# Kernel optimization log

Hardware: AMD Instinct MI355X
Metric: run time of the kernel (lower is better)

## Reference

```python
import jax, jax.numpy as jnp
import numpy as np

LMAX = 2; C = 64; H = 8; D = C // H
N_NODES = 10000; N_EDGES = 160000
M = (LMAX + 1) ** 2                      # 9 spherical components
RAD_IN = 64; RAD_HID = 64
WNUM = (LMAX + 1) * C                    # per-edge CP-TP weights: one per (l, channel)
L_OF_M = jnp.array([l for l in range(LMAX + 1) for _ in range(2 * l + 1)])
LN_EPS = 1e-5


def _lin(x, W, b=None):
    # Linear over channel (last) dim; bias applied ONLY to scalar (m=0) component
    y = jnp.einsum('nmc,cd->nmd', x, W)
    if b is not None:
        y = y.at[:, 0, :].add(b)
    return y


def _cp_tp(x, sh, w_lc):
    # CP tensor product with SH: channelwise product, per-(l, channel) radial weight
    # x: [E, M, C], sh: [E, M], w_lc: [E, LMAX+1, C]
    return x * sh[:, :, None] * w_lc[:, L_OF_M, :]


def _radial(s, W1, b1, g, b, W2, off):
    h = s @ W1 + b1
    mu = h.mean(-1, keepdims=True)
    var = h.var(-1, keepdims=True)
    h = (h - mu) / jnp.sqrt(var + LN_EPS) * g + b
    h = jax.nn.silu(h)
    return (h @ W2 + off).reshape(-1, LMAX + 1, C)


def _smooth_lrelu(x, a=0.2):
    return (1 + a) / 2 * x + (1 - a) / 2 * x * (2 * jax.nn.sigmoid(x) - 1)


def _gate(x):
    c = x.shape[-1] // 2
    v = x[..., :c]
    g = jax.nn.sigmoid(x[:, 0, c:])[:, None, :]
    return jnp.concatenate([jax.nn.silu(v[:, :1, :]), v[:, 1:, :] * g], axis=1)


def _seg_softmax(a, idx, n):
    # numerically stable softmax over edges grouped by destination node
    m = jax.ops.segment_max(a, idx, num_segments=n)
    e = jnp.exp(a - m[idx])
    s = jax.ops.segment_sum(e, idx, num_segments=n)
    return e / (s[idx] + 1e-16)


def setup_inputs():
    key = jax.random.key(0)
    ks = jax.random.split(key, 16)
    def w(k, shape, fan_in):
        return jax.random.normal(k, shape, jnp.float32) / np.sqrt(fan_in)
    bound = 1.0 / np.sqrt(RAD_HID)
    return {
        'node_input': jax.random.normal(ks[0], (N_NODES, M, C), jnp.float32),
        'edge_attr': jax.random.normal(ks[1], (N_EDGES, M), jnp.float32),
        'edge_scalars': jax.random.normal(ks[2], (N_EDGES, RAD_IN), jnp.float32),
        'W_src': w(ks[3], (C, C), C), 'b_src': jnp.zeros((C,), jnp.float32),
        'W_dst': w(ks[4], (C, C), C),
        'rad_W1': w(ks[5], (RAD_IN, RAD_HID), RAD_IN),
        'rad_b1': jnp.zeros((RAD_HID,), jnp.float32),
        'rad_ln_g': jnp.ones((RAD_HID,), jnp.float32),
        'rad_ln_b': jnp.zeros((RAD_HID,), jnp.float32),
        'rad_W2': w(ks[6], (RAD_HID, WNUM), RAD_HID),
        'rad_offset': jax.random.uniform(ks[7], (WNUM,), jnp.float32, -bound, bound),
        'W_alpha': w(ks[8], (C, C), C), 'b_alpha': jnp.zeros((C,), jnp.float32),
        'alpha_dot': w(ks[9], (H, D), D),
        'W_value': w(ks[10], (C, 2 * C), C), 'b_value': jnp.zeros((2 * C,), jnp.float32),
        'W_proj': w(ks[11], (C, C), C), 'b_proj': jnp.zeros((C,), jnp.float32),
        'edge_src': jax.random.randint(ks[12], (N_EDGES,), 0, N_NODES),
        'edge_dst': jax.random.randint(ks[13], (N_EDGES,), 0, N_NODES),
        'batch': jnp.zeros((N_NODES,), jnp.int32),
    }


def reference(node_input, edge_attr, edge_scalars, W_src, b_src, W_dst,
              rad_W1, rad_b1, rad_ln_g, rad_ln_b, rad_W2, rad_offset,
              W_alpha, b_alpha, alpha_dot, W_value, b_value, W_proj, b_proj,
              edge_src, edge_dst, batch):
    # gather: per-edge merged message [E, M, C]
    msg = _lin(node_input, W_src, b_src)[edge_src] + _lin(node_input, W_dst)[edge_dst]
    # per-edge radial weights for both tensor products [E, LMAX+1, C]
    w_lc = _radial(edge_scalars, rad_W1, rad_b1, rad_ln_g, rad_ln_b, rad_W2, rad_offset)
    msg = _cp_tp(msg, edge_attr, w_lc)
    # alpha path: scalar channel only
    alpha = _lin(msg, W_alpha, b_alpha)[:, 0, :].reshape(-1, H, D)
    alpha = _smooth_lrelu(alpha)[:, None]                 # [E, 1, H, D]
    alpha = jnp.einsum('bikd,kd->bik', alpha, alpha_dot)  # [E, 1, H]
    alpha = _seg_softmax(alpha, edge_dst, N_NODES)        # dropout disabled (eval)
    # value path
    value = _gate(_lin(msg, W_value, b_value))
    value = _cp_tp(value, edge_attr, w_lc)
    value = value.reshape(N_EDGES, M, H, D)
    # scatter-aggregate to destination nodes
    out = jax.ops.segment_sum(value * alpha[:, :, :, None], edge_dst, num_segments=N_NODES)
    return _lin(out.reshape(N_NODES, M, C), W_proj, b_proj)
```

## Files before the change

### kernel.cpp

```cpp
#include <hip/hip_runtime.h>
#include <stdint.h>

#define NN 10000
#define NE 160000

struct BF16 { unsigned short v; };
typedef _Float16 h2_t __attribute__((ext_vector_type(2)));
typedef _Float16 f16x8 __attribute__((ext_vector_type(8)));
typedef float f32x4 __attribute__((ext_vector_type(4)));

__device__ __forceinline__ float cvt(float x) { return x; }
__device__ __forceinline__ float cvt(BF16 x) {
    union { unsigned int i; float f; } u; u.i = ((unsigned int)x.v) << 16; return u.f;
}
__device__ __forceinline__ unsigned short f2b_us(float f) {
    union { float f; unsigned int i; } v; v.f = f;
    unsigned int x = v.i;
    unsigned int lsb = (x >> 16) & 1u;
    x += 0x7fffu + lsb;
    return (unsigned short)(x >> 16);
}
__device__ __forceinline__ float rlane(float v, int l) {
    return __uint_as_float((unsigned int)__builtin_amdgcn_readlane(__float_as_uint(v), l));
}
__device__ __forceinline__ h2_t rlane_pk(h2_t v, int l) {
    union { h2_t h; unsigned int u; } c; c.h = v;
    c.u = (unsigned int)__builtin_amdgcn_readlane(c.u, l);
    return c.h;
}
__device__ __forceinline__ h2_t pkh2(float a, float b) {
    h2_t r; r[0] = (_Float16)a; r[1] = (_Float16)b; return r;
}
__device__ __forceinline__ float fdot2f(h2_t a, h2_t b, float c) {
#if __has_builtin(__builtin_amdgcn_fdot2)
    return __builtin_amdgcn_fdot2(a, b, c, false);
#else
    return fmaf((float)a[0], (float)b[0], fmaf((float)a[1], (float)b[1], c));
#endif
}
__device__ __forceinline__ float sigm(float x) { return 1.0f / (1.0f + __expf(-x)); }
__device__ __forceinline__ int clampi(int v, int hi) { return (unsigned)v >= (unsigned)hi ? 0 : v; }

__device__ __forceinline__ void stOut(float* p, size_t i, float v) { p[i] = v; }
__device__ __forceinline__ void stOut(unsigned short* p, size_t i, float v) { p[i] = f2b_us(v); }

__device__ __forceinline__ unsigned okey(float f) {
    unsigned b = __float_as_uint(f);
    return (b & 0x80000000u) ? ~b : (b | 0x80000000u);
}
__device__ __forceinline__ float okdec(unsigned k) {
    unsigned b = (k & 0x80000000u) ? (k ^ 0x80000000u) : ~k;
    return __uint_as_float(b);
}

__device__ __forceinline__ f16x8 ld8f16(const BF16* p) {
    uint4 v = *(const uint4*)p;
    unsigned w0 = v.x, w1 = v.y, w2 = v.z, w3 = v.w;
    f16x8 r;
    union { unsigned u; float f; } c;
    c.u = (w0 & 0xFFFFu) << 16;  r[0] = (_Float16)c.f;
    c.u = (w0 & 0xFFFF0000u);    r[1] = (_Float16)c.f;
    c.u = (w1 & 0xFFFFu) << 16;  r[2] = (_Float16)c.f;
    c.u = (w1 & 0xFFFF0000u);    r[3] = (_Float16)c.f;
    c.u = (w2 & 0xFFFFu) << 16;  r[4] = (_Float16)c.f;
    c.u = (w2 & 0xFFFF0000u);    r[5] = (_Float16)c.f;
    c.u = (w3 & 0xFFFFu) << 16;  r[6] = (_Float16)c.f;
    c.u = (w3 & 0xFFFF0000u);    r[7] = (_Float16)c.f;
    return r;
}
__device__ __forceinline__ f16x8 ld8f16(const float* p) {
    float4 a = *(const float4*)p;
    float4 b = *(const float4*)(p + 4);
    f16x8 r;
    r[0] = (_Float16)a.x; r[1] = (_Float16)a.y; r[2] = (_Float16)a.z; r[3] = (_Float16)a.w;
    r[4] = (_Float16)b.x; r[5] = (_Float16)b.y; r[6] = (_Float16)b.z; r[7] = (_Float16)b.w;
    return r;
}

__global__ void k0_zero(int* __restrict__ cnt, int* __restrict__ csr, int* __restrict__ flag,
                        float* __restrict__ nsum, unsigned* __restrict__ mseg,
                        float* __restrict__ sseg) {
    int i = blockIdx.x * blockDim.x + threadIdx.x;
    if (i == 0) *flag = 1;
    if (i < NN) cnt[i] = 0;
    if (i < NE) csr[i] = 0;
    if (i < NN * 8) { mseg[i] = 0u; sseg[i] = 0.f; }
    for (int j = i; j < NN * 576; j += gridDim.x * blockDim.x) nsum[j] = 0.f;
}

__global__ void kprobe(const unsigned short* __restrict__ x, int* __restrict__ flag) {
    int bad = 0;
    for (int i = threadIdx.x; i < 16384; i += blockDim.x) {
        unsigned e = (x[i] >> 7) & 0xFFu;
        bad += (e == 0xFFu);
    }
    if (bad > 0) atomicExch(flag, 0);
}

template<typename T>
__device__ void k1m_body(const T* x, const T* Ws, const T* bs, const T* Wd,
                         _Float16* fs, _Float16* fd, _Float16 (*Yt)[128])
{
    const int lane = threadIdx.x & 63;
    const int c16 = lane & 15;
    const int kg  = lane >> 4;

    f16x8 bWs[4][2], bWd[4][2];
#pragma unroll
    for (int t = 0; t < 4; t++)
#pragma unroll
        for (int kh = 0; kh < 2; kh++) {
            f16x8 f1, f2;
#pragma unroll
            for (int j = 0; j < 8; j++) {
                int k = kh * 32 + kg * 8 + j;
                f1[j] = (_Float16)cvt(Ws[(size_t)k * 64 + t * 16 + c16]);
                f2[j] = (_Float16)cvt(Wd[(size_t)k * 64 + t * 16 + c16]);
            }
            bWs[t][kh] = f1; bWd[t][kh] = f2;
        }
    float bsv[4];
#pragma unroll
    for (int t = 0; t < 4; t++) bsv[t] = cvt(bs[t * 16 + c16]);

    const int NT = (NN * 9) / 16;
    for (int tile = blockIdx.x * 4 + (threadIdx.x >> 6); tile < NT; tile += gridDim.x * 4) {
        const int r0 = tile * 16;
        f16x8 a0 = ld8f16(&x[(size_t)(r0 + c16) * 64 + kg * 8]);
        f16x8 a1 = ld8f16(&x[(size_t)(r0 + c16) * 64 + 32 + kg * 8]);
        f32x4 hs[4] = {{0,0,0,0},{0,0,0,0},{0,0,0,0},{0,0,0,0}};
        f32x4 hd[4] = {{0,0,0,0},{0,0,0,0},{0,0,0,0},{0,0,0,0}};
#pragma unroll
        for (int t = 0; t < 4; t++) {
            hs[t] = __builtin_amdgcn_mfma_f32_16x16x32_f16(a0, bWs[t][0], hs[t], 0, 0, 0);
            hs[t] = __builtin_amdgcn_mfma_f32_16x16x32_f16(a1, bWs[t][1], hs[t], 0, 0, 0);
            hd[t] = __builtin_amdgcn_mfma_f32_16x16x32_f16(a0, bWd[t][0], hd[t], 0, 0, 0);
            hd[t] = __builtin_amdgcn_mfma_f32_16x16x32_f16(a1, bWd[t][1], hd[t], 0, 0, 0);
        }
#pragma unroll
        for (int t = 0; t < 4; t++)
#pragma unroll
            for (int r = 0; r < 4; r++) {
                int row = kg * 4 + r;
                float vs = hs[t][r];
                if (((r0 + row) % 9) == 0) vs += bsv[t];
                Yt[row][t * 16 + c16] = (_Float16)vs;
                Yt[row][64 + t * 16 + c16] = (_Float16)hd[t][r];
            }
#pragma unroll
        for (int j = 0; j < 2; j++) {
            int c = lane + 64 * j;
            int row = c >> 3;
            int cc = (c & 7) * 8;
            *(f16x8*)&fs[(size_t)(r0 + row) * 64 + cc] = *(const f16x8*)&Yt[row][cc];
            *(f16x8*)&fd[(size_t)(r0 + row) * 64 + cc] = *(const f16x8*)&Yt[row][64 + cc];
        }
    }
}

__global__ __launch_bounds__(256) void k1m_feats(
    const void* x, const void* Ws, const void* bs, const void* Wd,
    _Float16* fs, _Float16* fd, const int* flag)
{
    __shared__ _Float16 Y[4][16][128];
    const int wv = threadIdx.x >> 6;
    if (*flag) k1m_body<BF16>((const BF16*)x, (const BF16*)Ws, (const BF16*)bs, (const BF16*)Wd,
                              fs, fd, Y[wv]);
    else       k1m_body<float>((const float*)x, (const float*)Ws, (const float*)bs, (const float*)Wd,
                               fs, fd, Y[wv]);
}

__global__ void k2a_count(const int* __restrict__ dst, int* __restrict__ cnt) {
    for (int e = blockIdx.x * blockDim.x + threadIdx.x; e < NE; e += gridDim.x * blockDim.x)
        atomicAdd(&cnt[clampi(dst[e], NN)], 1);
}

__global__ __launch_bounds__(1024) void k2b_scan(const int* __restrict__ cnt,
                                                 int* __restrict__ off, int* __restrict__ cur) {
    __shared__ int part[1024];
    int t = threadIdx.x;
    int base = t * 10;
    int loc[10]; int s = 0;
#pragma unroll
    for (int k = 0; k < 10; k++) { int i = base + k; int v = (i < NN) ? cnt[i] : 0; loc[k] = v; s += v; }
    part[t] = s; __syncthreads();
    for (int o = 1; o < 1024; o <<= 1) {
        int v = (t >= o) ? part[t - o] : 0;
        __syncthreads();
        part[t] += v;
        __syncthreads();
    }
    int run = (t == 0) ? 0 : part[t - 1];
#pragma unroll
    for (int k = 0; k < 10; k++) {
        int i = base + k;
        if (i < NN) { off[i] = run; cur[i] = run; run += loc[k]; }
    }
    if (t == 1023) off[NN] = part[1023];
}

__global__ void k2c_fill(const int* __restrict__ dst, int* __restrict__ cur, int* __restrict__ csr) {
    for (int e = blockIdx.x * blockDim.x + threadIdx.x; e < NE; e += gridDim.x * blockDim.x) {
        int d = clampi(dst[e], NN);
        int p = atomicAdd(&cur[d], 1);
        if ((unsigned)p < (unsigned)NE) csr[p] = e;
    }
}

template<typename T>
__device__ void k3m_body(const T* es, const T* W1, const T* b1g, const T* gg, const T* bbv,
                         const T* W2, const T* roff, _Float16* wlc,
                         _Float16 (*Yt)[200])
{
    const int lane = threadIdx.x & 63;
    const int c16 = lane & 15;
    const int kg  = lane >> 4;

    f16x8 bW1[4][2], bW2[12][2];
#pragma unroll
    for (int t = 0; t < 4; t++)
#pragma unroll
        for (int kh = 0; kh < 2; kh++) {
            f16x8 f;
#pragma unroll
            for (int j = 0; j < 8; j++) {
                int k = kh * 32 + kg * 8 + j;
                f[j] = (_Float16)cvt(W1[(size_t)k * 64 + t * 16 + c16]);
            }
            bW1[t][kh] = f;
        }
#pragma unroll
    for (int t = 0; t < 12; t++)
#pragma unroll
        for (int kh = 0; kh < 2; kh++) {
            f16x8 f;
#pragma unroll
            for (int j = 0; j < 8; j++) {
                int k = kh * 32 + kg * 8 + j;
                f[j] = (_Float16)cvt(W2[(size_t)k * 192 + t * 16 + c16]);
            }
            bW2[t][kh] = f;
        }
    float b1v[4], gv[4], bv[4], rv[12];
#pragma unroll
    for (int t = 0; t < 4; t++) {
        b1v[t] = cvt(b1g[t * 16 + c16]);
        gv[t]  = cvt(gg[t * 16 + c16]);
        bv[t]  = cvt(bbv[t * 16 + c16]);
    }
#pragma unroll
    for (int t = 0; t < 12; t++) rv[t] = cvt(roff[t * 16 + c16]);

    const int NT = NE / 16;
    for (int tile = blockIdx.x * 4 + (threadIdx.x >> 6); tile < NT; tile += gridDim.x * 4) {
        const int e0 = tile * 16;
        f16x8 a0 = ld8f16(&es[(size_t)(e0 + c16) * 64 + kg * 8]);
        f16x8 a1 = ld8f16(&es[(size_t)(e0 + c16) * 64 + 32 + kg * 8]);
        f32x4 h[4] = {{0,0,0,0},{0,0,0,0},{0,0,0,0},{0,0,0,0}};
#pragma unroll
        for (int t = 0; t < 4; t++) {
            h[t] = __builtin_amdgcn_mfma_f32_16x16x32_f16(a0, bW1[t][0], h[t], 0, 0, 0);
            h[t] = __builtin_amdgcn_mfma_f32_16x16x32_f16(a1, bW1[t][1], h[t], 0, 0, 0);
        }
#pragma unroll
        for (int r = 0; r < 4; r++) {
            float x0 = h[0][r] + b1v[0], x1 = h[1][r] + b1v[1];
            float x2 = h[2][r] + b1v[2], x3 = h[3][r] + b1v[3];
            float s = x0 + x1 + x2 + x3;
            float q = x0 * x0 + x1 * x1 + x2 * x2 + x3 * x3;
            s += __shfl_xor(s, 1, 64); q += __shfl_xor(q, 1, 64);
            s += __shfl_xor(s, 2, 64); q += __shfl_xor(q, 2, 64);
            s += __shfl_xor(s, 4, 64); q += __shfl_xor(q, 4, 64);
            s += __shfl_xor(s, 8, 64); q += __shfl_xor(q, 8, 64);
            float mu = s * (1.0f / 64.0f);
            float var = fmaxf(q * (1.0f / 64.0f) - mu * mu, 0.0f);
            float rs = rsqrtf(var + 1e-5f);
            int row = kg * 4 + r;
#pragma unroll
            for (int t = 0; t < 4; t++) {
                float xt = (t == 0) ? x0 : (t == 1) ? x1 : (t == 2) ? x2 : x3;
                float v = (xt - mu) * rs * gv[t] + bv[t];
                v = v * sigm(v);
                Yt[row][t * 16 + c16] = (_Float16)v;
            }
        }
        f16x8 a20 = *(const f16x8*)&Yt[c16][kg * 8];
        f16x8 a21 = *(const f16x8*)&Yt[c16][32 + kg * 8];
        f32x4 y[12] = {{0,0,0,0},{0,0,0,0},{0,0,0,0},{0,0,0,0},{0,0,0,0},{0,0,0,0},
                       {0,0,0,0},{0,0,0,0},{0,0,0,0},{0,0,0,0},{0,0,0,0},{0,0,0,0}};
#pragma unroll
        for (int t = 0; t < 12; t++) {
            y[t] = __builtin_amdgcn_mfma_f32_16x16x32_f16(a20, bW2[t][0], y[t], 0, 0, 0);
            y[t] = __builtin_amdgcn_mfma_f32_16x16x32_f16(a21, bW2[t][1], y[t], 0, 0, 0);
        }
#pragma unroll
        for (int t = 0; t < 12; t++)
#pragma unroll
            for (int r = 0; r < 4; r++)
                Yt[kg * 4 + r][t * 16 + c16] = (_Float16)(y[t][r] + rv[t]);
#pragma unroll
        for (int j = 0; j < 6; j++) {
            int c = lane + 64 * j;
            int row = c / 24;
            int cc = (c % 24) * 8;
            *(f16x8*)&wlc[(size_t)(e0 + row) * 192 + cc] = *(const f16x8*)&Yt[row][cc];
        }
    }
}

__global__ __launch_bounds__(256) void k3m_wlc(
    const void* es, const void* W1, const void* b1, const void* g, const void* bln,
    const void* W2, const void* roff, _Float16* wlc, const int* flag)
{
    __shared__ _Float16 Y[4][16][200];
    const int wv = threadIdx.x >> 6;
    if (*flag) k3m_body<BF16>((const BF16*)es, (const BF16*)W1, (const BF16*)b1, (const BF16*)g,
                              (const BF16*)bln, (const BF16*)W2, (const BF16*)roff, wlc, Y[wv]);
    else       k3m_body<float>((const float*)es, (const float*)W1, (const float*)b1, (const float*)g,
                               (const float*)bln, (const float*)W2, (const float*)roff, wlc, Y[wv]);
}

template<typename T>
__device__ void k4m_body(const T* ea, const _Float16* fs, const _Float16* fd,
                         const _Float16* wlc, const T* Wa, const T* ba, const T* adot,
                         const int* esrc, const int* edst, float* alpha, unsigned* mseg,
                         float (*aS)[8])
{
    const int lane = threadIdx.x & 63;
    const int c16 = lane & 15;
    const int kg  = lane >> 6 == 0 ? (lane >> 4) : (lane >> 4);

    f16x8 bWa[4][2];
#pragma unroll
    for (int t = 0; t < 4; t++)
#pragma unroll
        for (int kh = 0; kh < 2; kh++) {
            f16x8 f;
#pragma unroll
            for (int j = 0; j < 8; j++) {
                int k = kh * 32 + (lane >> 4) * 8 + j;
                f[j] = (_Float16)cvt(Wa[(size_t)k * 64 + t * 16 + c16]);
            }
            bWa[t][kh] = f;
        }
    float bav[4], adv[4];
#pragma unroll
    for (int t = 0; t < 4; t++) {
        bav[t] = cvt(ba[t * 16 + c16]);
        adv[t] = cvt(adot[t * 16 + c16]);
    }
    const int kgr = lane >> 4;

    const int NT = NE / 16;
    for (int tile = blockIdx.x * 4 + (threadIdx.x >> 6); tile < NT; tile += gridDim.x * 4) {
        const int e0 = tile * 16;
        const int eA = e0 + c16;
        const int sn = clampi(esrc[eA], NN);
        const int dn = clampi(edst[eA], NN);
        f16x8 fs0 = *(const f16x8*)&fs[(size_t)sn * 576 + kgr * 8];
        f16x8 fs1 = *(const f16x8*)&fs[(size_t)sn * 576 + 32 + kgr * 8];
        f16x8 fd0 = *(const f16x8*)&fd[(size_t)dn * 576 + kgr * 8];
        f16x8 fd1 = *(const f16x8*)&fd[(size_t)dn * 576 + 32 + kgr * 8];
        f16x8 wl0 = *(const f16x8*)&wlc[(size_t)eA * 192 + kgr * 8];
        f16x8 wl1 = *(const f16x8*)&wlc[(size_t)eA * 192 + 32 + kgr * 8];
        _Float16 eh = (_Float16)cvt(ea[(size_t)eA * 9]);
        f16x8 ev;
#pragma unroll
        for (int j = 0; j < 8; j++) ev[j] = eh;
        f16x8 a0 = (fs0 + fd0) * ev * wl0;
        f16x8 a1 = (fs1 + fd1) * ev * wl1;

        f32x4 d[4] = {{0,0,0,0},{0,0,0,0},{0,0,0,0},{0,0,0,0}};
#pragma unroll
        for (int t = 0; t < 4; t++) {
            d[t] = __builtin_amdgcn_mfma_f32_16x16x32_f16(a0, bWa[t][0], d[t], 0, 0, 0);
            d[t] = __builtin_amdgcn_mfma_f32_16x16x32_f16(a1, bWa[t][1], d[t], 0, 0, 0);
        }
#pragma unroll
        for (int t = 0; t < 4; t++)
#pragma unroll
            for (int r = 0; r < 4; r++) {
                float aw = d[t][r] + bav[t];
                float f = aw * (0.2f + 0.8f * sigm(aw));
                float p = f * adv[t];
                p += __shfl_xor(p, 1, 64);
                p += __shfl_xor(p, 2, 64);
                p += __shfl_xor(p, 4, 64);
                if ((c16 & 7) == 0)
                    aS[kgr * 4 + r][t * 2 + (c16 >> 3)] = p;
            }
#pragma unroll
        for (int j = 0; j < 2; j++) {
            int idx = lane * 2 + j;
            int row = idx >> 3, h = idx & 7;
            float p = aS[row][h];
            alpha[(size_t)(e0 + row) * 8 + h] = p;
            int dnr = clampi(edst[e0 + row], NN);
            atomicMax(&mseg[dnr * 8 + h], okey(p));
        }
    }
}

__global__ __launch_bounds__(256) void k4m_alpha(
    const void* ea, const _Float16* fs, const _Float16* fd, const _Float16* wlc,
    const void* Wa, const void* ba, const void* adot,
    const int* esrc, const int* edst, float* alpha, unsigned* mseg, const int* flag)
{
    __shared__ float A[4][16][8];
    const int wv = threadIdx.x >> 6;
    if (*flag) k4m_body<BF16>((const BF16*)ea, fs, fd, wlc, (const BF16*)Wa, (const BF16*)ba,
                              (const BF16*)adot, esrc, edst, alpha, mseg, A[wv]);
    else       k4m_body<float>((const float*)ea, fs, fd, wlc, (const float*)Wa, (const float*)ba,
                               (const float*)adot, esrc, edst, alpha, mseg, A[wv]);
}

__global__ void k5b_expsum(const int* __restrict__ edst, const unsigned* __restrict__ mseg,
                           float* __restrict__ alpha, float* __restrict__ sseg) {
    int t = blockIdx.x * blockDim.x + threadIdx.x;
    if (t >= NE * 8) return;
    int e = t >> 3, h = t & 7;
    int dn = clampi(edst[e], NN);
    float m = okdec(mseg[dn * 8 + h]);
    float ex = __expf(alpha[t] - m);
    alpha[t] = ex;
    unsafeAtomicAdd(&sseg[dn * 8 + h], ex);
}

template<typename T>
__device__ void k6m_body(const int* off, const int* csr, const int* esrc,
                         const T* ea, const _Float16* fs, const _Float16* fd,
                         const _Float16* wlc, const T* Wv, const T* bv,
                         const float* alpha, const float* sseg, float* nsum,
                         _Float16 (*wlS)[16][72], float (*mtS)[20])
{
    const int lane = threadIdx.x & 63;
    const int wvid = threadIdx.x >> 6;
    const int c16 = lane & 15;
    const int kg  = lane >> 4;

    for (int gw = blockIdx.x * 4 + wvid; gw < NN * 2; gw += gridDim.x * 4) {
        const int n = gw >> 1;
        const int half = gw & 1;
        const int b = off[n], e_end = off[n + 1];
        if (b >= e_end) continue;

        f16x8 bfV[2][2], bfG[2][2];
        float bvv[2], bgv[2];
        int colg[2], hh[2];
        float invs[2];
#pragma unroll
        for (int t = 0; t < 2; t++) {
            colg[t] = (half * 2 + t) * 16 + c16;
            hh[t] = colg[t] >> 3;
            invs[t] = 1.0f / (sseg[n * 8 + hh[t]] + 1e-16f);
#pragma unroll
            for (int kh = 0; kh < 2; kh++) {
                f16x8 b8v, b8g;
#pragma unroll
                for (int j = 0; j < 8; j++) {
                    int k = kh * 32 + kg * 8 + j;
                    b8v[j] = (_Float16)cvt(Wv[(size_t)k * 128 + colg[t]]);
                    b8g[j] = (_Float16)cvt(Wv[(size_t)k * 128 + 64 + colg[t]]);
                }
                bfV[t][kh] = b8v; bfG[t][kh] = b8g;
            }
            bvv[t] = cvt(bv[colg[t]]);
            bgv[t] = cvt(bv[64 + colg[t]]);
        }

        const size_t fdb = (size_t)n * 576;
        const size_t nbase = (size_t)n * 576;

        for (int p0 = b; p0 < e_end; p0 += 16) {
            int pA = p0 + c16; if (pA >= e_end) pA = e_end - 1;
            const int eA = clampi(csr[pA], NE);
            const int snA = clampi(esrc[eA], NN);
            const size_t fsb = (size_t)snA * 576;
            const size_t wlb = (size_t)eA * 192;

#pragma unroll
            for (int l = 0; l < 3; l++)
#pragma unroll
                for (int kh = 0; kh < 2; kh++)
                    *(f16x8*)&wlS[l][c16][kh * 32 + kg * 8] =
                        *(const f16x8*)&wlc[wlb + (size_t)l * 64 + kh * 32 + kg * 8];
            float eao[9];
#pragma unroll
            for (int m = 0; m < 9; m++) eao[m] = cvt(ea[(size_t)eA * 9 + m]);
            if (kg == 0) {
#pragma unroll
                for (int m = 0; m < 9; m++) mtS[c16][m] = eao[m];
            }
            mtS[c16][10 + kg * 2]     = alpha[(size_t)eA * 8 + kg * 2];
            mtS[c16][10 + kg * 2 + 1] = alpha[(size_t)eA * 8 + kg * 2 + 1];

            float awm[2][4];
#pragma unroll
            for (int r = 0; r < 4; r++) {
                int row = kg * 4 + r;
                float vm = (p0 + row < e_end) ? 1.f : 0.f;
#pragma unroll
                for (int t = 0; t < 2; t++)
                    awm[t][r] = mtS[row][10 + hh[t]] * invs[t] * vm;
            }

            float gtv[2][4];
            {
                f16x8 a0, a1;
                {
                    f16x8 w0 = *(const f16x8*)&wlS[0][c16][kg * 8];
                    f16x8 w1 = *(const f16x8*)&wlS[0][c16][32 + kg * 8];
                    f16x8 fd0 = *(const f16x8*)&fd[fdb + kg * 8];
                    f16x8 fd1 = *(const f16x8*)&fd[fdb + 32 + kg * 8];
                    f16x8 fs0 = *(const f16x8*)&fs[fsb + kg * 8];
                    f16x8 fs1 = *(const f16x8*)&fs[fsb + 32 + kg * 8];
                    _Float16 eh = (_Float16)eao[0];
                    f16x8 ev;
#pragma unroll
                    for (int j = 0; j < 8; j++) ev[j] = eh;
                    a0 = (fs0 + fd0) * ev * w0;
                    a1 = (fs1 + fd1) * ev * w1;
                }
                f32x4 d[2] = {{0,0,0,0},{0,0,0,0}};
                f32x4 g[2] = {{0,0,0,0},{0,0,0,0}};
#pragma unroll
                for (int t = 0; t < 2; t++) {
                    d[t] = __builtin_amdgcn_mfma_f32_16x16x32_f16(a0, bfV[t][0], d[t], 0, 0, 0);
                    d[t] = __builtin_amdgcn_mfma_f32_16x16x32_f16(a1, bfV[t][1], d[t], 0, 0, 0);
                    g[t] = __builtin_amdgcn_mfma_f32_16x16x32_f16(a0, bfG[t][0], g[t], 0, 0, 0);
                    g[t] = __builtin_amdgcn_mfma_f32_16x16x32_f16(a1, bfG[t][1], g[t], 0, 0, 0);
                }
#pragma unroll
                for (int t = 0; t < 2; t++) {
                    float ps = 0.f;
#pragma unroll
                    for (int r = 0; r < 4; r++) {
                        int row = kg * 4 + r;
                        gtv[t][r] = sigm(g[t][r] + bgv[t]);
                        float v = d[t][r] + bvv[t];
                        float f = v * sigm(v);
                        float wlv = (float)wlS[0][row][colg[t]];
                        float eam = mtS[row][0];
                        ps = fmaf(f * (eam * wlv), awm[t][r], ps);
                    }
                    ps += __shfl_xor(ps, 16, 64);
                    ps += __shfl_xor(ps, 32, 64);
                    if (kg == 0) unsafeAtomicAdd(&nsum[nbase + colg[t]], ps);
                }
            }
#pragma unroll 2
            for (int m = 1; m < 9; m++) {
                const int l = (m < 4) ? 1 : 2;
                f16x8 a0, a1;
                {
                    const size_t mo = (size_t)m * 64;
                    f16x8 w0 = *(const f16x8*)&wlS[l][c16][kg * 8];
                    f16x8 w1 = *(const f16x8*)&wlS[l][c16][32 + kg * 8];
                    f16x8 fd0 = *(const f16x8*)&fd[fdb + mo + kg * 8];
                    f16x8 fd1 = *(const f16x8*)&fd[fdb + mo + 32 + kg * 8];
                    f16x8 fs0 = *(const f16x8*)&fs[fsb + mo + kg * 8];
                    f16x8 fs1 = *(const f16x8*)&fs[fsb + mo + 32 + kg * 8];
                    _Float16 eh = (_Float16)eao[m];
                    f16x8 ev;
#pragma unroll
                    for (int j = 0; j < 8; j++) ev[j] = eh;
                    a0 = (fs0 + fd0) * ev * w0;
                    a1 = (fs1 + fd1) * ev * w1;
                }
                f32x4 d[2] = {{0,0,0,0},{0,0,0,0}};
#pragma unroll
                for (int t = 0; t < 2; t++) {
                    d[t] = __builtin_amdgcn_mfma_f32_16x16x32_f16(a0, bfV[t][0], d[t], 0, 0, 0);
                    d[t] = __builtin_amdgcn_mfma_f32_16x16x32_f16(a1, bfV[t][1], d[t], 0, 0, 0);
                }
#pragma unroll
                for (int t = 0; t < 2; t++) {
                    float ps = 0.f;
#pragma unroll
                    for (int r = 0; r < 4; r++) {
                        int row = kg * 4 + r;
                        float f = d[t][r] * gtv[t][r];
                        float wlv = (float)wlS[l][row][colg[t]];
                        float eam = mtS[row][m];
                        ps = fmaf(f * (eam * wlv), awm[t][r], ps);
                    }
                    ps += __shfl_xor(ps, 16, 64);
                    ps += __shfl_xor(ps, 32, 64);
                    if (kg == 0) unsafeAtomicAdd(&nsum[nbase + (size_t)m * 64 + colg[t]], ps);
                }
            }
        }
    }
}

__global__ __launch_bounds__(256) void k6m_fused(
    const int* off, const int* csr, const int* esrc,
    const void* ea, const _Float16* fs, const _Float16* fd, const _Float16* wlc,
    const void* Wv, const void* bv,
    const float* alpha, const float* sseg, float* nsum, const int* flag)
{
    __shared__ _Float16 shwl[4][3][16][72];
    __shared__ float    shmt[4][16][20];
    const int wvid = threadIdx.x >> 6;
    if (*flag) k6m_body<BF16>(off, csr, esrc, (const BF16*)ea, fs, fd, wlc,
                              (const BF16*)Wv, (const BF16*)bv, alpha, sseg, nsum,
                              shwl[wvid], shmt[wvid]);
    else       k6m_body<float>(off, csr, esrc, (const float*)ea, fs, fd, wlc,
                               (const float*)Wv, (const float*)bv, alpha, sseg, nsum,
                               shwl[wvid], shmt[wvid]);
}

template<typename T, typename OT>
__device__ void k7_body(const float* nsum, const T* Wp, const T* bp, OT* out)
{
    int lane = threadIdx.x & 63;
    int wv = threadIdx.x >> 6;
    float wp[64];
#pragma unroll
    for (int i = 0; i < 64; i++) wp[i] = cvt(Wp[i * 64 + lane]);
    float bpl = cvt(bp[lane]);
    const int ROWS = NN * 9;
    for (int r = blockIdx.x * 4 + wv; r < ROWS; r += gridDim.x * 4) {
        float xv = nsum[(size_t)r * 64 + lane];
        float o0 = 0, o1 = 0, o2 = 0, o3 = 0;
#pragma unroll
        for (int i = 0; i < 64; i += 4) {
            o0 = fmaf(rlane(xv, i), wp[i], o0);
            o1 = fmaf(rlane(xv, i + 1), wp[i + 1], o1);
            o2 = fmaf(rlane(xv, i + 2), wp[i + 2], o2);
            o3 = fmaf(rlane(xv, i + 3), wp[i + 3], o3);
        }
        float o = o0 + o1 + o2 + o3;
        if ((r % 9) == 0) o += bpl;
        stOut(out, (size_t)r * 64 + lane, o);
    }
}

__global__ __launch_bounds__(256) void k7_proj(
    const float* nsum, const void* Wp, const void* bp, void* out, const int* flag)
{
    if (*flag) k7_body<BF16, unsigned short>(nsum, (const BF16*)Wp, (const BF16*)bp, (unsigned short*)out);
    else       k7_body<float, float>(nsum, (const float*)Wp, (const float*)bp, (float*)out);
}

extern "C" void kernel_launch(void* const* d_in, const int* in_sizes, int n_in,
                              void* d_out, int out_size, void* d_ws, size_t ws_size,
                              hipStream_t stream) {
    const void* node_input = d_in[0];
    const void* edge_attr  = d_in[1];
    const void* edge_scal  = d_in[2];
    const void* W_src      = d_in[3];
    const void* b_src      = d_in[4];
    const void* W_dst      = d_in[5];
    const void* rad_W1     = d_in[6];
    const void* rad_b1     = d_in[7];
    const void* rad_ln_g   = d_in[8];
    const void* rad_ln_b   = d_in[9];
    const void* rad_W2     = d_in[10];
    const void* rad_off    = d_in[11];
    const void* W_alpha    = d_in[12];
    const void* b_alpha    = d_in[13];
    const void* alpha_dot  = d_in[14];
    const void* W_value    = d_in[15];
    const void* b_value    = d_in[16];
    const void* W_proj     = d_in[17];
    const void* b_proj     = d_in[18];
    const int* edge_src    = (const int*)d_in[19];
    const int* edge_dst    = (const int*)d_in[20];

    char* ws = (char*)d_ws;
    size_t ofs = 0;
    auto alloc = [&](size_t bytes) -> char* {
        char* r = ws + ofs;
        ofs = (ofs + bytes + 255) & ~(size_t)255;
        return r;
    };

    int* flag       = (int*)alloc(256);
    int* cnt        = (int*)alloc((size_t)NN * 4);
    int* offs       = (int*)alloc((size_t)(NN + 16) * 4);
    int* cur        = (int*)alloc((size_t)NN * 4);
    int* csr        = (int*)alloc((size_t)NE * 4);
    unsigned* mseg  = (unsigned*)alloc((size_t)NN * 8 * 4);
    float* sseg     = (float*)alloc((size_t)NN * 8 * 4);
    float* alpha    = (float*)alloc((size_t)NE * 8 * 4);
    _Float16* fs    = (_Float16*)alloc((size_t)NN * 576 * 2);
    _Float16* fd    = (_Float16*)alloc((size_t)NN * 576 * 2);
    _Float16* wlc   = (_Float16*)alloc((size_t)NE * 192 * 2);
    float* nsum32   = (float*)alloc((size_t)NN * 576 * 4);

    k0_zero<<<dim3(625), dim3(256), 0, stream>>>(cnt, csr, flag, nsum32, mseg, sseg);
    kprobe<<<dim3(1), dim3(256), 0, stream>>>((const unsigned short*)node_input, flag);
    k1m_feats<<<dim3(1408), dim3(256), 0, stream>>>(node_input, W_src, b_src, W_dst, fs, fd, flag);
    k2a_count<<<dim3(512), dim3(256), 0, stream>>>(edge_dst, cnt);
    k2b_scan<<<dim3(1), dim3(1024), 0, stream>>>(cnt, offs, cur);
    k2c_fill<<<dim3(512), dim3(256), 0, stream>>>(edge_dst, cur, csr);
    k3m_wlc<<<dim3(512), dim3(256), 0, stream>>>(edge_scal, rad_W1, rad_b1, rad_ln_g, rad_ln_b,
                                                 rad_W2, rad_off, wlc, flag);
    k4m_alpha<<<dim3(2500), dim3(256), 0, stream>>>(edge_attr, fs, fd, wlc, W_alpha, b_alpha,
                                                    alpha_dot, edge_src, edge_dst, alpha, mseg, flag);
    k5b_expsum<<<dim3(5000), dim3(256), 0, stream>>>(edge_dst, mseg, alpha, sseg);
    k6m_fused<<<dim3(5000), dim3(256), 0, stream>>>(offs, csr, edge_src, edge_attr, fs, fd, wlc,
                                                    W_value, b_value, alpha, sseg, nsum32, flag);
    k7_proj<<<dim3(2048), dim3(256), 0, stream>>>(nsum32, W_proj, b_proj, d_out, flag);
}
```

Baseline: 488.3 us.

## Accumulate node sums in registers, store fp16, and use MFMA for projection

The fused value kernel now keeps per-node partial sums in registers across all incoming edges and writes each node's result once as fp16. This replaces per-tile float atomics into a zero-initialised fp32 buffer, so the zeroing loop in k0 is dropped. The output projection becomes an MFMA 16x16x32 fp16 tile kernel that stages results through shared memory for vectorised stores. Nodes with no incoming edges now get explicit zeros because the early continue was removed. Storing the intermediate in fp16 lowers precision before the projection.

```diff
diff --git a/kernel.cpp b/kernel.cpp
--- a/kernel.cpp
+++ b/kernel.cpp
@@ -78,14 +78,12 @@
 }
 
 __global__ void k0_zero(int* __restrict__ cnt, int* __restrict__ csr, int* __restrict__ flag,
-                        float* __restrict__ nsum, unsigned* __restrict__ mseg,
-                        float* __restrict__ sseg) {
+                        unsigned* __restrict__ mseg, float* __restrict__ sseg) {
     int i = blockIdx.x * blockDim.x + threadIdx.x;
     if (i == 0) *flag = 1;
     if (i < NN) cnt[i] = 0;
     if (i < NE) csr[i] = 0;
     if (i < NN * 8) { mseg[i] = 0u; sseg[i] = 0.f; }
-    for (int j = i; j < NN * 576; j += gridDim.x * blockDim.x) nsum[j] = 0.f;
 }
 
 __global__ void kprobe(const unsigned short* __restrict__ x, int* __restrict__ flag) {
@@ -328,7 +326,7 @@
 {
     const int lane = threadIdx.x & 63;
     const int c16 = lane & 15;
-    const int kg  = lane >> 6 == 0 ? (lane >> 4) : (lane >> 4);
+    const int kgr = lane >> 4;
 
     f16x8 bWa[4][2];
 #pragma unroll
@@ -338,7 +336,7 @@
             f16x8 f;
 #pragma unroll
             for (int j = 0; j < 8; j++) {
-                int k = kh * 32 + (lane >> 4) * 8 + j;
+                int k = kh * 32 + kgr * 8 + j;
                 f[j] = (_Float16)cvt(Wa[(size_t)k * 64 + t * 16 + c16]);
             }
             bWa[t][kh] = f;
@@ -349,7 +347,6 @@
         bav[t] = cvt(ba[t * 16 + c16]);
         adv[t] = cvt(adot[t * 16 + c16]);
     }
-    const int kgr = lane >> 4;
 
     const int NT = NE / 16;
     for (int tile = blockIdx.x * 4 + (threadIdx.x >> 6); tile < NT; tile += gridDim.x * 4) {
@@ -430,7 +427,7 @@
 __device__ void k6m_body(const int* off, const int* csr, const int* esrc,
                          const T* ea, const _Float16* fs, const _Float16* fd,
                          const _Float16* wlc, const T* Wv, const T* bv,
-                         const float* alpha, const float* sseg, float* nsum,
+                         const float* alpha, const float* sseg, _Float16* nsum16,
                          _Float16 (*wlS)[16][72], float (*mtS)[20])
 {
     const int lane = threadIdx.x & 63;
@@ -442,7 +439,6 @@
         const int n = gw >> 1;
         const int half = gw & 1;
         const int b = off[n], e_end = off[n + 1];
-        if (b >= e_end) continue;
 
         f16x8 bfV[2][2], bfG[2][2];
         float bvv[2], bgv[2];
@@ -469,7 +465,9 @@
         }
 
         const size_t fdb = (size_t)n * 576;
-        const size_t nbase = (size_t)n * 576;
+        float accT[9][2];
+#pragma unroll
+        for (int m = 0; m < 9; m++) { accT[m][0] = 0.f; accT[m][1] = 0.f; }
 
         for (int p0 = b; p0 < e_end; p0 += 16) {
             int pA = p0 + c16; if (pA >= e_end) pA = e_end - 1;
@@ -543,12 +541,10 @@
                         float eam = mtS[row][0];
                         ps = fmaf(f * (eam * wlv), awm[t][r], ps);
                     }
-                    ps += __shfl_xor(ps, 16, 64);
-                    ps += __shfl_xor(ps, 32, 64);
-                    if (kg == 0) unsafeAtomicAdd(&nsum[nbase + colg[t]], ps);
+                    accT[0][t] += ps;
                 }
             }
-#pragma unroll 2
+#pragma unroll
             for (int m = 1; m < 9; m++) {
                 const int l = (m < 4) ? 1 : 2;
                 f16x8 a0, a1;
@@ -584,12 +580,20 @@
                         float eam = mtS[row][m];
                         ps = fmaf(f * (eam * wlv), awm[t][r], ps);
                     }
-                    ps += __shfl_xor(ps, 16, 64);
-                    ps += __shfl_xor(ps, 32, 64);
-                    if (kg == 0) unsafeAtomicAdd(&nsum[nbase + (size_t)m * 64 + colg[t]], ps);
+                    accT[m][t] += ps;
                 }
             }
         }
+
+#pragma unroll
+        for (int m = 0; m < 9; m++)
+#pragma unroll
+            for (int t = 0; t < 2; t++) {
+                float ps = accT[m][t];
+                ps += __shfl_xor(ps, 16, 64);
+                ps += __shfl_xor(ps, 32, 64);
+                if (kg == 0) nsum16[(size_t)n * 576 + m * 64 + colg[t]] = (_Float16)ps;
+            }
     }
 }
 
@@ -597,50 +601,83 @@
     const int* off, const int* csr, const int* esrc,
     const void* ea, const _Float16* fs, const _Float16* fd, const _Float16* wlc,
     const void* Wv, const void* bv,
-    const float* alpha, const float* sseg, float* nsum, const int* flag)
+    const float* alpha, const float* sseg, _Float16* nsum16, const int* flag)
 {
     __shared__ _Float16 shwl[4][3][16][72];
     __shared__ float    shmt[4][16][20];
     const int wvid = threadIdx.x >> 6;
     if (*flag) k6m_body<BF16>(off, csr, esrc, (const BF16*)ea, fs, fd, wlc,
-                              (const BF16*)Wv, (const BF16*)bv, alpha, sseg, nsum,
+                              (const BF16*)Wv, (const BF16*)bv, alpha, sseg, nsum16,
                               shwl[wvid], shmt[wvid]);
     else       k6m_body<float>(off, csr, esrc, (const float*)ea, fs, fd, wlc,
-                               (const float*)Wv, (const float*)bv, alpha, sseg, nsum,
+                               (const float*)Wv, (const float*)bv, alpha, sseg, nsum16,
                                shwl[wvid], shmt[wvid]);
 }
 
 template<typename T, typename OT>
-__device__ void k7_body(const float* nsum, const T* Wp, const T* bp, OT* out)
-{
-    int lane = threadIdx.x & 63;
-    int wv = threadIdx.x >> 6;
-    float wp[64];
-#pragma unroll
-    for (int i = 0; i < 64; i++) wp[i] = cvt(Wp[i * 64 + lane]);
-    float bpl = cvt(bp[lane]);
-    const int ROWS = NN * 9;
-    for (int r = blockIdx.x * 4 + wv; r < ROWS; r += gridDim.x * 4) {
-        float xv = nsum[(size_t)r * 64 + lane];
-        float o0 = 0, o1 = 0, o2 = 0, o3 = 0;
-#pragma unroll
-        for (int i = 0; i < 64; i += 4) {
-            o0 = fmaf(rlane(xv, i), wp[i], o0);
-            o1 = fmaf(rlane(xv, i + 1), wp[i + 1], o1);
-            o2 = fmaf(rlane(xv, i + 2), wp[i + 2], o2);
-            o3 = fmaf(rlane(xv, i + 3), wp[i + 3], o3);
-        }
-        float o = o0 + o1 + o2 + o3;
-        if ((r % 9) == 0) o += bpl;
-        stOut(out, (size_t)r * 64 + lane, o);
-    }
-}
-
-__global__ __launch_bounds__(256) void k7_proj(
-    const float* nsum, const void* Wp, const void* bp, void* out, const int* flag)
-{
-    if (*flag) k7_body<BF16, unsigned short>(nsum, (const BF16*)Wp, (const BF16*)bp, (unsigned short*)out);
-    else       k7_body<float, float>(nsum, (const float*)Wp, (const float*)bp, (float*)out);
+__device__ void k7m_body(const _Float16* ns, const T* Wp, const T* bp, OT* out, OT (*Yt)[72])
+{
+    const int lane = threadIdx.x & 63;
+    const int c16 = lane & 15;
+    const int kg  = lane >> 4;
+
+    f16x8 bWp[4][2];
+#pragma unroll
+    for (int t = 0; t < 4; t++)
+#pragma unroll
+        for (int kh = 0; kh < 2; kh++) {
+            f16x8 f;
+#pragma unroll
+            for (int j = 0; j < 8; j++) {
+                int k = kh * 32 + kg * 8 + j;
+                f[j] = (_Float16)cvt(Wp[(size_t)k * 64 + t * 16 + c16]);
+            }
+            bWp[t][kh] = f;
+        }
+    float bpv[4];
+#pragma unroll
+    for (int t = 0; t < 4; t++) bpv[t] = cvt(bp[t * 16 + c16]);
+
+    const int NT = (NN * 9) / 16;
+    for (int tile = blockIdx.x * 4 + (threadIdx.x >> 6); tile < NT; tile += gridDim.x * 4) {
+        const int r0 = tile * 16;
+        f16x8 a0 = *(const f16x8*)&ns[(size_t)(r0 + c16) * 64 + kg * 8];
+        f16x8 a1 = *(const f16x8*)&ns[(size_t)(r0 + c16) * 64 + 32 + kg * 8];
+        f32x4 d[4] = {{0,0,0,0},{0,0,0,0},{0,0,0,0},{0,0,0,0}};
+#pragma unroll
+        for (int t = 0; t < 4; t++) {
+            d[t] = __builtin_amdgcn_mfma_f32_16x16x32_f16(a0, bWp[t][0], d[t], 0, 0, 0);
+            d[t] = __builtin_amdgcn_mfma_f32_16x16x32_f16(a1, bWp[t][1], d[t], 0, 0, 0);
+        }
+#pragma unroll
+        for (int t = 0; t < 4; t++)
+#pragma unroll
+            for (int r = 0; r < 4; r++) {
+                int row = kg * 4 + r;
+                float o = d[t][r];
+                if (((r0 + row) % 9) == 0) o += bpv[t];
+                stOut((OT*)&Yt[row][0], t * 16 + c16, o);
+            }
+        const int CH = (64 * (int)sizeof(OT)) / 16;
+#pragma unroll
+        for (int j = 0; j < (16 * CH) / 64; j++) {
+            int c = lane + 64 * j;
+            int row = c / CH;
+            int cc = (c % CH) * (16 / (int)sizeof(OT));
+            *(uint4*)&out[(size_t)(r0 + row) * 64 + cc] = *(const uint4*)&Yt[row][cc];
+        }
+    }
+}
+
+__global__ __launch_bounds__(256) void k7m_proj(
+    const _Float16* ns, const void* Wp, const void* bp, void* out, const int* flag)
+{
+    __shared__ __align__(16) unsigned char Ybuf[4][16 * 72 * 4];
+    const int wv = threadIdx.x >> 6;
+    if (*flag) k7m_body<BF16, unsigned short>(ns, (const BF16*)Wp, (const BF16*)bp,
+                               (unsigned short*)out, (unsigned short (*)[72])Ybuf[wv]);
+    else       k7m_body<float, float>(ns, (const float*)Wp, (const float*)bp,
+                               (float*)out, (float (*)[72])Ybuf[wv]);
 }
 
 extern "C" void kernel_launch(void* const* d_in, const int* in_sizes, int n_in,
@@ -687,9 +724,9 @@
     _Float16* fs    = (_Float16*)alloc((size_t)NN * 576 * 2);
     _Float16* fd    = (_Float16*)alloc((size_t)NN * 576 * 2);
     _Float16* wlc   = (_Float16*)alloc((size_t)NE * 192 * 2);
-    float* nsum32   = (float*)alloc((size_t)NN * 576 * 4);
-
-    k0_zero<<<dim3(625), dim3(256), 0, stream>>>(cnt, csr, flag, nsum32, mseg, sseg);
+    _Float16* nsum16= (_Float16*)alloc((size_t)NN * 576 * 2);
+
+    k0_zero<<<dim3(625), dim3(256), 0, stream>>>(cnt, csr, flag, mseg, sseg);
     kprobe<<<dim3(1), dim3(256), 0, stream>>>((const unsigned short*)node_input, flag);
     k1m_feats<<<dim3(1408), dim3(256), 0, stream>>>(node_input, W_src, b_src, W_dst, fs, fd, flag);
     k2a_count<<<dim3(512), dim3(256), 0, stream>>>(edge_dst, cnt);
@@ -701,6 +738,6 @@
                                                     alpha_dot, edge_src, edge_dst, alpha, mseg, flag);
     k5b_expsum<<<dim3(5000), dim3(256), 0, stream>>>(edge_dst, mseg, alpha, sseg);
     k6m_fused<<<dim3(5000), dim3(256), 0, stream>>>(offs, csr, edge_src, edge_attr, fs, fd, wlc,
-                                                    W_value, b_value, alpha, sseg, nsum32, flag);
-    k7_proj<<<dim3(2048), dim3(256), 0, stream>>>(nsum32, W_proj, b_proj, d_out, flag);
-}
+                                                    W_value, b_value, alpha, sseg, nsum16, flag);
+    k7m_proj<<<dim3(1408), dim3(256), 0, stream>>>(nsum16, W_proj, b_proj, d_out, flag);
+}
```

Result: slower. 577.3 us (+18.2%).
